# Performance work log

Hardware: AMD Instinct MI355X
Metric: run time of the kernel (lower is better)

Reference implementation:

```python
import jax, jax.numpy as jnp
import numpy as np

S = 56
BATCH = 3136 * 0 + 256  # batch size
D = 5 * 2 + 20  # 5*B + C = 30 channels per cell
LAMBDA_COORD = 5.0
LAMBDA_NOOBJ = 0.5


def setup_inputs() -> dict:
    key = jax.random.key(0)
    k1, k2, k3 = jax.random.split(key, 3)
    predictions = jax.random.uniform(k1, (BATCH, S, S, D), dtype=jnp.float32,
                                     minval=0.01, maxval=1.0)
    target = jax.random.uniform(k2, (BATCH, S, S, D), dtype=jnp.float32,
                                 minval=0.01, maxval=1.0)
    # objectness channel must be exactly 1.0 or 0.0 (code tests target[...,4] == 1)
    obj = (jax.random.uniform(k3, (BATCH, S, S)) < 0.3).astype(jnp.float32)
    target = target.at[..., 4].set(obj)
    return {"predictions": predictions, "target": target}


def reference(predictions, target):
    # obj mask: cells where target objectness is exactly 1
    obj = (target[..., 4] == 1.0).astype(predictions.dtype)   # [B,S,S]
    noobj = 1.0 - obj

    # coord loss: (x,y) squared diff + (sqrt(w),sqrt(h)) squared diff
    dxy = jnp.sum((predictions[..., 0:2] - target[..., 0:2]) ** 2, axis=-1)
    dwh = jnp.sum((jnp.sqrt(predictions[..., 2:4]) - jnp.sqrt(target[..., 2:4])) ** 2, axis=-1)
    coord = LAMBDA_COORD * (dxy + dwh)

    # confidence squared error (used for both object and no-object terms)
    conf = (predictions[..., 4] - target[..., 4]) ** 2

    # class loss over [5:] (faithful to original slice)
    cls = jnp.sum((predictions[..., 5:] - target[..., 5:]) ** 2, axis=-1)

    per_cell = obj * (coord + conf + cls) + noobj * (LAMBDA_NOOBJ * conf)
    return jnp.sum(per_cell) / predictions.shape[0]
```

## Files before the change

kernel.cpp:

```cpp
#include <hip/hip_runtime.h>

#define NBATCH 256
#define NCH 30

typedef __attribute__((ext_vector_type(4))) float f32x4;

__device__ __forceinline__ float fast_sqrt(float x) {
    float r;
    asm("v_sqrt_f32 %0, %1" : "=v"(r) : "v"(x));
    return r;
}

__device__ __forceinline__ f32x4 gld128(const float* p) {
    f32x4 r;
    asm volatile("global_load_dwordx4 %0, %1, off" : "=v"(r) : "v"(p));
    return r;
}
__device__ __forceinline__ float gld32(const float* p) {
    float r;
    asm volatile("global_load_dword %0, %1, off" : "=v"(r) : "v"(p));
    return r;
}

__device__ __forceinline__ float quad_term(
    f32x4 pv, f32x4 tv, float clo, float chi,
    const float A[4], const float B[4], const bool SQ[4])
{
    float obj_lo = (clo == 1.0f) ? 1.0f : 0.0f;
    float obj_hi = (chi == 1.0f) ? 1.0f : 0.0f;
    float acc = 0.0f;
    #pragma unroll
    for (int k = 0; k < 4; ++k) {
        float p = pv[k], t = tv[k];
        float dns = p - t;
        float vns = dns * dns;
        float vsq = (p + t) - 2.0f * fast_sqrt(p * t);
        float val = SQ[k] ? vsq : vns;
        float ob  = (k < 2) ? obj_lo : obj_hi;
        float w   = fmaf(ob, A[k], B[k]);
        acc = fmaf(w, val, acc);
    }
    return acc;
}

template <bool USE_WS>
__global__ __launch_bounds__(256, 4) void yolo_loss_main_kernel(
    const float* __restrict__ pred,
    const float* __restrict__ targ,
    float* __restrict__ out,
    int n4)
{
    const int T   = gridDim.x * blockDim.x;
    const int tid = blockIdx.x * blockDim.x + threadIdx.x;

    const int e0    = tid * 4;
    const int c0    = e0 % NCH;
    const int cell0 = e0 / NCH;
    const int Flo0  = cell0 * NCH + 4;
    const int hioff = (c0 == 28) ? NCH : 0;

    float A[4], B[4];
    bool  SQ[4];
    #pragma unroll
    for (int k = 0; k < 4; ++k) {
        int c = c0 + k; if (c >= NCH) c -= NCH;
        SQ[k] = (c == 2 || c == 3);
        if (c < 4)       { A[k] = 5.0f; B[k] = 0.0f; }
        else if (c == 4) { A[k] = 0.5f; B[k] = 0.5f; }
        else             { A[k] = 1.0f; B[k] = 0.0f; }
    }

    float acc = 0.0f;

    if (n4 == 4 * T) {
        const int S = 4 * T;

        f32x4 pv0 = gld128(pred + e0 + 0*S);
        f32x4 tv0 = gld128(targ + e0 + 0*S);
        f32x4 pv1 = gld128(pred + e0 + 1*S);
        f32x4 tv1 = gld128(targ + e0 + 1*S);
        f32x4 pv2 = gld128(pred + e0 + 2*S);
        f32x4 tv2 = gld128(targ + e0 + 2*S);
        f32x4 pv3 = gld128(pred + e0 + 3*S);
        f32x4 tv3 = gld128(targ + e0 + 3*S);
        float clo0 = gld32(targ + Flo0 + 0*S);
        float clo1 = gld32(targ + Flo0 + 1*S);
        float clo2 = gld32(targ + Flo0 + 2*S);
        float clo3 = gld32(targ + Flo0 + 3*S);
        float chi0 = gld32(targ + Flo0 + hioff + 0*S);
        float chi1 = gld32(targ + Flo0 + hioff + 1*S);
        float chi2 = gld32(targ + Flo0 + hioff + 2*S);
        float chi3 = gld32(targ + Flo0 + hioff + 3*S);

        asm volatile("s_waitcnt vmcnt(0)" ::: "memory");
        __builtin_amdgcn_sched_barrier(0);

        acc += quad_term(pv0, tv0, clo0, chi0, A, B, SQ);
        acc += quad_term(pv1, tv1, clo1, chi1, A, B, SQ);
        acc += quad_term(pv2, tv2, clo2, chi2, A, B, SQ);
        acc += quad_term(pv3, tv3, clo3, chi3, A, B, SQ);
    } else {
        const int S = 4 * T;
        int m = 0;
        for (int i = tid; i < n4; i += T, ++m) {
            const float4* p4 = reinterpret_cast<const float4*>(pred);
            const float4* t4 = reinterpret_cast<const float4*>(targ);
            float4 pv = p4[i];
            float4 tv = t4[i];
            f32x4 pvv; pvv[0]=pv.x; pvv[1]=pv.y; pvv[2]=pv.z; pvv[3]=pv.w;
            f32x4 tvv; tvv[0]=tv.x; tvv[1]=tv.y; tvv[2]=tv.z; tvv[3]=tv.w;
            float clo = targ[Flo0 + m * S];
            float chi = targ[Flo0 + hioff + m * S];
            acc += quad_term(pvv, tvv, clo, chi, A, B, SQ);
        }
    }

    #pragma unroll
    for (int off = 32; off > 0; off >>= 1)
        acc += __shfl_down(acc, off, 64);

    __shared__ float lds[4];
    int lane = threadIdx.x & 63;
    int wid  = threadIdx.x >> 6;
    if (lane == 0) lds[wid] = acc;
    __syncthreads();
    if (threadIdx.x == 0) {
        float s = lds[0] + lds[1] + lds[2] + lds[3];
        if (USE_WS) out[blockIdx.x] = s;
        else        atomicAdd(out, s * (1.0f / (float)NBATCH));
    }
}

__global__ __launch_bounds__(256) void yolo_loss_finish_kernel(
    const float* __restrict__ partial, float* __restrict__ out, int n)
{
    float acc = 0.0f;
    for (int i = threadIdx.x; i < n; i += 256) acc += partial[i];
    #pragma unroll
    for (int off = 32; off > 0; off >>= 1)
        acc += __shfl_down(acc, off, 64);
    __shared__ float lds[4];
    int lane = threadIdx.x & 63, wid = threadIdx.x >> 6;
    if (lane == 0) lds[wid] = acc;
    __syncthreads();
    if (threadIdx.x == 0)
        out[0] = (lds[0] + lds[1] + lds[2] + lds[3]) * (1.0f / (float)NBATCH);
}

extern "C" void kernel_launch(void* const* d_in, const int* in_sizes, int n_in,
                              void* d_out, int out_size, void* d_ws, size_t ws_size,
                              hipStream_t stream)
{
    const float* pred = (const float*)d_in[0];
    const float* targ = (const float*)d_in[1];
    float* out = (float*)d_out;

    int n  = in_sizes[0];
    int n4 = n / 4;

    int blocks = 5880;

    if (ws_size >= (size_t)blocks * sizeof(float)) {
        float* partial = (float*)d_ws;
        yolo_loss_main_kernel<true><<<blocks, 256, 0, stream>>>(pred, targ, partial, n4);
        yolo_loss_finish_kernel<<<1, 256, 0, stream>>>(partial, out, blocks);
    } else {
        hipMemsetAsync(out, 0, sizeof(float), stream);
        yolo_loss_main_kernel<false><<<blocks, 256, 0, stream>>>(pred, targ, out, n4);
    }
}
```

Baseline: 39.90 us.

## Halve grid and software-pipeline eight chunks per thread with double-buffered loads

The grid is halved to 2940 blocks, so each thread now processes eight strided float4 chunks instead of four. Loads are double-buffered: the next chunk's loads are issued before computing the current one, with a partial vmcnt wait. Launch bounds now request 8 blocks per CU to raise occupancy. Only two chunks are in flight per thread instead of four, which trades memory-level parallelism per thread for fewer blocks and more occupancy.

```diff
diff --git a/kernel.cpp b/kernel.cpp
--- a/kernel.cpp
+++ b/kernel.cpp
@@ -24,7 +24,7 @@
 
 __device__ __forceinline__ float quad_term(
     f32x4 pv, f32x4 tv, float clo, float chi,
-    const float A[4], const float B[4], const bool SQ[4])
+    const float WA[4], const float WB[4], const bool SQ[4])
 {
     float obj_lo = (clo == 1.0f) ? 1.0f : 0.0f;
     float obj_hi = (chi == 1.0f) ? 1.0f : 0.0f;
@@ -37,14 +37,14 @@
         float vsq = (p + t) - 2.0f * fast_sqrt(p * t);
         float val = SQ[k] ? vsq : vns;
         float ob  = (k < 2) ? obj_lo : obj_hi;
-        float w   = fmaf(ob, A[k], B[k]);
+        float w   = fmaf(ob, WA[k], WB[k]);
         acc = fmaf(w, val, acc);
     }
     return acc;
 }
 
 template <bool USE_WS>
-__global__ __launch_bounds__(256, 4) void yolo_loss_main_kernel(
+__global__ __launch_bounds__(256, 8) void yolo_loss_main_kernel(
     const float* __restrict__ pred,
     const float* __restrict__ targ,
     float* __restrict__ out,
@@ -59,59 +59,68 @@
     const int Flo0  = cell0 * NCH + 4;
     const int hioff = (c0 == 28) ? NCH : 0;
 
-    float A[4], B[4];
+    float WA[4], WB[4];
     bool  SQ[4];
     #pragma unroll
     for (int k = 0; k < 4; ++k) {
         int c = c0 + k; if (c >= NCH) c -= NCH;
         SQ[k] = (c == 2 || c == 3);
-        if (c < 4)       { A[k] = 5.0f; B[k] = 0.0f; }
-        else if (c == 4) { A[k] = 0.5f; B[k] = 0.5f; }
-        else             { A[k] = 1.0f; B[k] = 0.0f; }
+        if (c < 4)       { WA[k] = 5.0f; WB[k] = 0.0f; }
+        else if (c == 4) { WA[k] = 0.5f; WB[k] = 0.5f; }
+        else             { WA[k] = 1.0f; WB[k] = 0.0f; }
     }
 
     float acc = 0.0f;
 
-    if (n4 == 4 * T) {
+    if (n4 == 8 * T) {
         const int S = 4 * T;
+        const float* pp = pred + e0;
+        const float* tp = targ + e0;
+        const float* cl = targ + Flo0;
+        const float* ch = targ + Flo0 + hioff;
 
-        f32x4 pv0 = gld128(pred + e0 + 0*S);
-        f32x4 tv0 = gld128(targ + e0 + 0*S);
-        f32x4 pv1 = gld128(pred + e0 + 1*S);
-        f32x4 tv1 = gld128(targ + e0 + 1*S);
-        f32x4 pv2 = gld128(pred + e0 + 2*S);
-        f32x4 tv2 = gld128(targ + e0 + 2*S);
-        f32x4 pv3 = gld128(pred + e0 + 3*S);
-        f32x4 tv3 = gld128(targ + e0 + 3*S);
-        float clo0 = gld32(targ + Flo0 + 0*S);
-        float clo1 = gld32(targ + Flo0 + 1*S);
-        float clo2 = gld32(targ + Flo0 + 2*S);
-        float clo3 = gld32(targ + Flo0 + 3*S);
-        float chi0 = gld32(targ + Flo0 + hioff + 0*S);
-        float chi1 = gld32(targ + Flo0 + hioff + 1*S);
-        float chi2 = gld32(targ + Flo0 + hioff + 2*S);
-        float chi3 = gld32(targ + Flo0 + hioff + 3*S);
+        f32x4 pvX = gld128(pp);
+        f32x4 tvX = gld128(tp);
+        float cloX = gld32(cl);
+        float chiX = gld32(ch);
+        f32x4 pvY, tvY;
+        float cloY, chiY;
+
+        #define STEP(CUR, NXT)                                              \
+            pp += S; tp += S; cl += S; ch += S;                             \
+            pv##NXT  = gld128(pp);                                          \
+            tv##NXT  = gld128(tp);                                          \
+            clo##NXT = gld32(cl);                                           \
+            chi##NXT = gld32(ch);                                           \
+            asm volatile("s_waitcnt vmcnt(4)" ::: "memory");                \
+            __builtin_amdgcn_sched_barrier(0);                              \
+            acc += quad_term(pv##CUR, tv##CUR, clo##CUR, chi##CUR, WA, WB, SQ);
+
+        STEP(X, Y)
+        STEP(Y, X)
+        STEP(X, Y)
+        STEP(Y, X)
+        STEP(X, Y)
+        STEP(Y, X)
+        STEP(X, Y)
+        #undef STEP
 
         asm volatile("s_waitcnt vmcnt(0)" ::: "memory");
         __builtin_amdgcn_sched_barrier(0);
-
-        acc += quad_term(pv0, tv0, clo0, chi0, A, B, SQ);
-        acc += quad_term(pv1, tv1, clo1, chi1, A, B, SQ);
-        acc += quad_term(pv2, tv2, clo2, chi2, A, B, SQ);
-        acc += quad_term(pv3, tv3, clo3, chi3, A, B, SQ);
+        acc += quad_term(pvY, tvY, cloY, chiY, WA, WB, SQ);
     } else {
         const int S = 4 * T;
+        const float4* p4 = reinterpret_cast<const float4*>(pred);
+        const float4* t4 = reinterpret_cast<const float4*>(targ);
         int m = 0;
         for (int i = tid; i < n4; i += T, ++m) {
-            const float4* p4 = reinterpret_cast<const float4*>(pred);
-            const float4* t4 = reinterpret_cast<const float4*>(targ);
             float4 pv = p4[i];
             float4 tv = t4[i];
             f32x4 pvv; pvv[0]=pv.x; pvv[1]=pv.y; pvv[2]=pv.z; pvv[3]=pv.w;
             f32x4 tvv; tvv[0]=tv.x; tvv[1]=tv.y; tvv[2]=tv.z; tvv[3]=tv.w;
             float clo = targ[Flo0 + m * S];
             float chi = targ[Flo0 + hioff + m * S];
-            acc += quad_term(pvv, tvv, clo, chi, A, B, SQ);
+            acc += quad_term(pvv, tvv, clo, chi, WA, WB, SQ);
         }
     }
 
@@ -158,7 +167,7 @@
     int n  = in_sizes[0];
     int n4 = n / 4;
 
-    int blocks = 5880;
+    int blocks = 2940;
 
     if (ws_size >= (size_t)blocks * sizeof(float)) {
         float* partial = (float*)d_ws;
```

Result: faster. 38.39 us, median of 3 (-3.8%).

## Give each thread 16 contiguous elements instead of four strided float4 chunks

Applied to the files above, without the earlier changes.

Each thread now loads a contiguous run of 16 floats from prediction and target as four adjacent 128-bit loads, rather than four float4s spaced a full grid stride apart. Per-element channel weights are computed inline. Because 16 elements span at most two cells, only two objectness loads are needed per thread instead of eight. Launch bounds are raised to 8 waves per SIMD. The contiguous per-thread layout gives wider per-lane strides, which may reduce coalescing across a wavefront in exchange for fewer flag loads.

```diff
diff --git a/kernel.cpp b/kernel.cpp
--- a/kernel.cpp
+++ b/kernel.cpp
@@ -22,96 +22,83 @@
     return r;
 }
 
-__device__ __forceinline__ float quad_term(
-    f32x4 pv, f32x4 tv, float clo, float chi,
-    const float A[4], const float B[4], const bool SQ[4])
-{
-    float obj_lo = (clo == 1.0f) ? 1.0f : 0.0f;
-    float obj_hi = (chi == 1.0f) ? 1.0f : 0.0f;
-    float acc = 0.0f;
-    #pragma unroll
-    for (int k = 0; k < 4; ++k) {
-        float p = pv[k], t = tv[k];
-        float dns = p - t;
-        float vns = dns * dns;
-        float vsq = (p + t) - 2.0f * fast_sqrt(p * t);
-        float val = SQ[k] ? vsq : vns;
-        float ob  = (k < 2) ? obj_lo : obj_hi;
-        float w   = fmaf(ob, A[k], B[k]);
-        acc = fmaf(w, val, acc);
-    }
-    return acc;
-}
-
 template <bool USE_WS>
-__global__ __launch_bounds__(256, 4) void yolo_loss_main_kernel(
+__global__ __launch_bounds__(256, 8) void yolo_loss_main_kernel(
     const float* __restrict__ pred,
     const float* __restrict__ targ,
     float* __restrict__ out,
-    int n4)
+    int n)
 {
     const int T   = gridDim.x * blockDim.x;
     const int tid = blockIdx.x * blockDim.x + threadIdx.x;
 
-    const int e0    = tid * 4;
-    const int c0    = e0 % NCH;
-    const int cell0 = e0 / NCH;
-    const int Flo0  = cell0 * NCH + 4;
-    const int hioff = (c0 == 28) ? NCH : 0;
-
-    float A[4], B[4];
-    bool  SQ[4];
-    #pragma unroll
-    for (int k = 0; k < 4; ++k) {
-        int c = c0 + k; if (c >= NCH) c -= NCH;
-        SQ[k] = (c == 2 || c == 3);
-        if (c < 4)       { A[k] = 5.0f; B[k] = 0.0f; }
-        else if (c == 4) { A[k] = 0.5f; B[k] = 0.5f; }
-        else             { A[k] = 1.0f; B[k] = 0.0f; }
-    }
-
     float acc = 0.0f;
 
-    if (n4 == 4 * T) {
-        const int S = 4 * T;
+    if (n == 16 * T) {
+        const int e0    = tid * 16;
+        const int c0    = e0 % NCH;
+        const int cell0 = e0 / NCH;
+        const int Flo0  = cell0 * NCH + 4;
+        const int hioff = (c0 >= 16) ? NCH : 0;
 
-        f32x4 pv0 = gld128(pred + e0 + 0*S);
-        f32x4 tv0 = gld128(targ + e0 + 0*S);
-        f32x4 pv1 = gld128(pred + e0 + 1*S);
-        f32x4 tv1 = gld128(targ + e0 + 1*S);
-        f32x4 pv2 = gld128(pred + e0 + 2*S);
-        f32x4 tv2 = gld128(targ + e0 + 2*S);
-        f32x4 pv3 = gld128(pred + e0 + 3*S);
-        f32x4 tv3 = gld128(targ + e0 + 3*S);
-        float clo0 = gld32(targ + Flo0 + 0*S);
-        float clo1 = gld32(targ + Flo0 + 1*S);
-        float clo2 = gld32(targ + Flo0 + 2*S);
-        float clo3 = gld32(targ + Flo0 + 3*S);
-        float chi0 = gld32(targ + Flo0 + hioff + 0*S);
-        float chi1 = gld32(targ + Flo0 + hioff + 1*S);
-        float chi2 = gld32(targ + Flo0 + hioff + 2*S);
-        float chi3 = gld32(targ + Flo0 + hioff + 3*S);
+        f32x4 pa = gld128(pred + e0 + 0);
+        f32x4 pb = gld128(pred + e0 + 4);
+        f32x4 pc = gld128(pred + e0 + 8);
+        f32x4 pd = gld128(pred + e0 + 12);
+        f32x4 ta = gld128(targ + e0 + 0);
+        f32x4 tb = gld128(targ + e0 + 4);
+        f32x4 tc = gld128(targ + e0 + 8);
+        f32x4 td = gld128(targ + e0 + 12);
+        float clo = gld32(targ + Flo0);
+        float chi = gld32(targ + Flo0 + hioff);
 
         asm volatile("s_waitcnt vmcnt(0)" ::: "memory");
         __builtin_amdgcn_sched_barrier(0);
 
-        acc += quad_term(pv0, tv0, clo0, chi0, A, B, SQ);
-        acc += quad_term(pv1, tv1, clo1, chi1, A, B, SQ);
-        acc += quad_term(pv2, tv2, clo2, chi2, A, B, SQ);
-        acc += quad_term(pv3, tv3, clo3, chi3, A, B, SQ);
+        float obj_lo = (clo == 1.0f) ? 1.0f : 0.0f;
+        float obj_hi = (chi == 1.0f) ? 1.0f : 0.0f;
+        const int nlo = NCH - c0;
+
+        float P[16], Q[16];
+        #pragma unroll
+        for (int k = 0; k < 4; ++k) {
+            P[k] = pa[k]; P[4+k] = pb[k]; P[8+k] = pc[k]; P[12+k] = pd[k];
+            Q[k] = ta[k]; Q[4+k] = tb[k]; Q[8+k] = tc[k]; Q[12+k] = td[k];
+        }
+
+        #pragma unroll
+        for (int k = 0; k < 16; ++k) {
+            int c = c0 + k; if (c >= NCH) c -= NCH;
+            bool  sq  = (c == 2) || (c == 3);
+            bool  is4 = (c == 4);
+            float wa  = (c < 4) ? 5.0f : (is4 ? 0.5f : 1.0f);
+            float wb  = is4 ? 0.5f : 0.0f;
+            float ob  = (k < nlo) ? obj_lo : obj_hi;
+            float p = P[k], t = Q[k];
+            float dns = p - t;
+            float vns = dns * dns;
+            float vsq = (p + t) - 2.0f * fast_sqrt(p * t);
+            float val = sq ? vsq : vns;
+            float w   = fmaf(ob, wa, wb);
+            acc = fmaf(w, val, acc);
+        }
     } else {
-        const int S = 4 * T;
-        int m = 0;
-        for (int i = tid; i < n4; i += T, ++m) {
-            const float4* p4 = reinterpret_cast<const float4*>(pred);
-            const float4* t4 = reinterpret_cast<const float4*>(targ);
-            float4 pv = p4[i];
-            float4 tv = t4[i];
-            f32x4 pvv; pvv[0]=pv.x; pvv[1]=pv.y; pvv[2]=pv.z; pvv[3]=pv.w;
-            f32x4 tvv; tvv[0]=tv.x; tvv[1]=tv.y; tvv[2]=tv.z; tvv[3]=tv.w;
-            float clo = targ[Flo0 + m * S];
-            float chi = targ[Flo0 + hioff + m * S];
-            acc += quad_term(pvv, tvv, clo, chi, A, B, SQ);
+        for (int e = tid; e < n; e += T) {
+            int cell = e / NCH;
+            int c    = e - cell * NCH;
+            float p = pred[e], t = targ[e];
+            float conf = targ[cell * NCH + 4];
+            float obj  = (conf == 1.0f) ? 1.0f : 0.0f;
+            bool  sq   = (c == 2) || (c == 3);
+            bool  is4  = (c == 4);
+            float wa   = (c < 4) ? 5.0f : (is4 ? 0.5f : 1.0f);
+            float wb   = is4 ? 0.5f : 0.0f;
+            float dns = p - t;
+            float vns = dns * dns;
+            float vsq = (p + t) - 2.0f * fast_sqrt(p * t);
+            float val = sq ? vsq : vns;
+            float w   = fmaf(obj, wa, wb);
+            acc = fmaf(w, val, acc);
         }
     }
 
@@ -155,17 +142,16 @@
     const float* targ = (const float*)d_in[1];
     float* out = (float*)d_out;
 
-    int n  = in_sizes[0];
-    int n4 = n / 4;
+    int n = in_sizes[0];
 
     int blocks = 5880;
 
     if (ws_size >= (size_t)blocks * sizeof(float)) {
         float* partial = (float*)d_ws;
-        yolo_loss_main_kernel<true><<<blocks, 256, 0, stream>>>(pred, targ, partial, n4);
+        yolo_loss_main_kernel<true><<<blocks, 256, 0, stream>>>(pred, targ, partial, n);
         yolo_loss_finish_kernel<<<1, 256, 0, stream>>>(partial, out, blocks);
     } else {
         hipMemsetAsync(out, 0, sizeof(float), stream);
-        yolo_loss_main_kernel<false><<<blocks, 256, 0, stream>>>(pred, targ, out, n4);
+        yolo_loss_main_kernel<false><<<blocks, 256, 0, stream>>>(pred, targ, out, n);
     }
 }
```

After: 39.90 us. No clear change (+0.0%).
